# Kernel tuning notes

Measured on AMD Instinct MI355X. Metric: run time of the kernel, lower is better.

## Reference

```python
import jax, jax.numpy as jnp
import numpy as np

B, N, F, H = 4, 512, 64, 128
EPS = 0.0            # GINE eps (train_eps=False)
NEG_SLOPE = 0.01     # leaky_relu negative slope


def setup_inputs() -> dict:
    key = jax.random.key(0)
    ks = jax.random.split(key, 8)
    x = jax.random.normal(ks[0], (B, N, F), dtype=jnp.float32)
    adj = jax.random.uniform(ks[1], (B, N, N), dtype=jnp.float32)
    edge_attr = jax.random.normal(ks[2], (B, N, N, F), dtype=jnp.float32)
    mask = jax.random.randint(ks[3], (B, N), 0, 2) > 0  # bool (B,N)
    W1 = jax.random.normal(ks[4], (F, H), dtype=jnp.float32) / np.sqrt(F)
    b1 = jnp.zeros((H,), dtype=jnp.float32)
    W2 = jax.random.normal(ks[5], (H, F), dtype=jnp.float32) / np.sqrt(H)
    b2 = jnp.zeros((F,), dtype=jnp.float32)
    return {"x": x, "adj": adj, "edge_attr": edge_attr, "mask": mask,
            "W1": W1, "b1": b1, "W2": W2, "b2": b2}


def reference(x, adj, edge_attr, mask, W1, b1, W2, b2):
    # z[b,i,j,f] = x[b,i,f] + edge_attr[b,i,j,f]
    # msg = leaky_relu(adj[b,i,j] * z); aggregate over source axis i (dim 1)
    msg = jax.nn.leaky_relu(adj[..., None] * (x[:, :, None, :] + edge_attr),
                            negative_slope=NEG_SLOPE)
    agg = jnp.sum(msg, axis=1)                      # (B, N, F), indexed by j
    out = (1.0 + EPS) * x + agg                     # add_loop=True
    # nn applied on masked rows, zeros elsewhere (equivalent to out[mask]=nn(out[mask]))
    h = jax.nn.leaky_relu(out @ W1 + b1, negative_slope=NEG_SLOPE) @ W2 + b2
    return jnp.where(mask[..., None], h, jnp.zeros((), dtype=h.dtype))
```

## Files before the change

kernel.cpp:

```cpp
#include <hip/hip_runtime.h>


namespace {

constexpr int Bc = 4;
constexpr int Nc = 512;
constexpr int Fc = 64;
constexpr int Hc = 128;
constexpr int TJ = 4;
constexpr int TH = 512;
constexpr float NEG = 0.01f;

__device__ __forceinline__ float lrelu(float z) {
  return z > 0.f ? z : z * NEG;
}

__global__ __launch_bounds__(TH, 4) void gine_fused(
    const float* __restrict__ x,
    const float* __restrict__ adj,
    const float* __restrict__ ea,
    const int* __restrict__ mask,
    const float* __restrict__ W1,
    const float* __restrict__ b1,
    const float* __restrict__ W2,
    const float* __restrict__ b2,
    float* __restrict__ out)
{
  const int blk = blockIdx.x;
  const int b   = blk >> 7;
  const int j0  = (blk & 127) * TJ;
  const int tid = threadIdx.x;
  const int f4  = tid & 15;
  const int jl  = (tid >> 4) & 3;
  const int ip  = tid >> 6;

  __shared__ float4 s_adj4[Nc];
  __shared__ float4 s_part[TH];
  __shared__ float  s_out[TJ][Fc];
  __shared__ float  s_hid[TJ][Hc];

  const float* adjb = adj + (size_t)b * Nc * Nc;
  s_adj4[tid] = *reinterpret_cast<const float4*>(adjb + (size_t)tid * Nc + j0);
  __syncthreads();

  const float4* xb4 = reinterpret_cast<const float4*>(x + (size_t)b * Nc * Fc);
  const float4* eap = reinterpret_cast<const float4*>(ea)
                    + ((size_t)b * Nc * Nc + (j0 + jl)) * (Fc / 4) + f4;
  constexpr int ISTRIDE = Nc * Fc / 4;

  float4 acc = make_float4(0.f, 0.f, 0.f, 0.f);
  #pragma unroll 4
  for (int i = ip; i < Nc; i += 8) {
    const float a   = reinterpret_cast<const float*>(&s_adj4[i])[jl];
    const float4 xv = xb4[i * (Fc / 4) + f4];
    const float4 ev = eap[(size_t)i * ISTRIDE];
    acc.x += lrelu(a * (xv.x + ev.x));
    acc.y += lrelu(a * (xv.y + ev.y));
    acc.z += lrelu(a * (xv.z + ev.z));
    acc.w += lrelu(a * (xv.w + ev.w));
  }

  s_part[tid] = acc;
  __syncthreads();
  #pragma unroll
  for (int s = 256; s >= 64; s >>= 1) {
    if (tid < s) {
      float4 p = s_part[tid];
      const float4 q = s_part[tid + s];
      p.x += q.x; p.y += q.y; p.z += q.z; p.w += q.w;
      s_part[tid] = p;
    }
    __syncthreads();
  }

  if (tid < 64) {
    const int row = tid >> 4;
    const int fg  = tid & 15;
    float4 r = s_part[tid];
    const float4 xj = xb4[(j0 + row) * (Fc / 4) + fg];
    r.x += xj.x; r.y += xj.y; r.z += xj.z; r.w += xj.w;
    reinterpret_cast<float4*>(&s_out[row][0])[fg] = r;
  }
  __syncthreads();

  {
    const int row = tid >> 7;
    const int h   = tid & 127;
    float hv = b1[h];
    #pragma unroll 8
    for (int f = 0; f < Fc; ++f)
      hv = fmaf(s_out[row][f], W1[f * Hc + h], hv);
    s_hid[row][h] = lrelu(hv);
  }
  __syncthreads();

  if (tid < TJ * Fc) {
    const int row = tid >> 6;
    const int f   = tid & 63;
    float o = b2[f];
    #pragma unroll 8
    for (int h = 0; h < Hc; ++h)
      o = fmaf(s_hid[row][h], W2[h * Fc + f], o);
    const int rowg = b * Nc + j0 + row;
    out[rowg * Fc + f] = (mask[rowg] != 0) ? o : 0.f;
  }
}

}

extern "C" void kernel_launch(void* const* d_in, const int* in_sizes, int n_in,
                              void* d_out, int out_size, void* d_ws, size_t ws_size,
                              hipStream_t stream) {
  const float* x    = (const float*)d_in[0];
  const float* adj  = (const float*)d_in[1];
  const float* ea   = (const float*)d_in[2];
  const int*   mask = (const int*)d_in[3];
  const float* W1   = (const float*)d_in[4];
  const float* b1   = (const float*)d_in[5];
  const float* W2   = (const float*)d_in[6];
  const float* b2   = (const float*)d_in[7];
  float* out = (float*)d_out;

  gine_fused<<<dim3(Bc * Nc / TJ), dim3(TH), 0, stream>>>(
      x, adj, ea, mask, W1, b1, W2, b2, out);
}
```

Baseline: 378.4 us.

## Widen destination tile to eight columns with nontemporal edge loads

Doubles the number of destination columns per block (TJ 4→8). Each thread now handles 8 features as two float4 loads per source row, and the edge_attr stream uses nontemporal loads. The intent is to cut per-block overhead (adjacency staging, reduction, MLP tail), issue more memory traffic per thread, and keep the edge stream from polluting the cache. In exchange the grid halves to 256 blocks, so fewer waves are available to hide memory latency on a large GPU. Leaky-relu also becomes a branchless max.

```diff
diff --git a/kernel.cpp b/kernel.cpp
--- a/kernel.cpp
+++ b/kernel.cpp
@@ -7,15 +7,27 @@
 constexpr int Nc = 512;
 constexpr int Fc = 64;
 constexpr int Hc = 128;
-constexpr int TJ = 4;
+constexpr int TJ = 8;
 constexpr int TH = 512;
 constexpr float NEG = 0.01f;
 
+typedef float f4 __attribute__((ext_vector_type(4)));
+
 __device__ __forceinline__ float lrelu(float z) {
-  return z > 0.f ? z : z * NEG;
+  return fmaxf(z, z * NEG);
 }
 
-__global__ __launch_bounds__(TH, 4) void gine_fused(
+__device__ __forceinline__ f4 lrelu4(f4 z) {
+  f4 zn = z * NEG;
+  f4 r;
+  r.x = fmaxf(z.x, zn.x);
+  r.y = fmaxf(z.y, zn.y);
+  r.z = fmaxf(z.z, zn.z);
+  r.w = fmaxf(z.w, zn.w);
+  return r;
+}
+
+__global__ __launch_bounds__(TH, 2) void gine_fused(
     const float* __restrict__ x,
     const float* __restrict__ adj,
     const float* __restrict__ ea,
@@ -27,82 +39,100 @@
     float* __restrict__ out)
 {
   const int blk = blockIdx.x;
-  const int b   = blk >> 7;
-  const int j0  = (blk & 127) * TJ;
+  const int b   = blk >> 6;
+  const int j0  = (blk & 63) * TJ;
   const int tid = threadIdx.x;
-  const int f4  = tid & 15;
-  const int jl  = (tid >> 4) & 3;
+  const int f8  = tid & 7;
+  const int jl  = (tid >> 3) & 7;
   const int ip  = tid >> 6;
 
-  __shared__ float4 s_adj4[Nc];
-  __shared__ float4 s_part[TH];
-  __shared__ float  s_out[TJ][Fc];
-  __shared__ float  s_hid[TJ][Hc];
+  __shared__ float s_adj[Nc][TJ];
+  __shared__ f4    s_pA[TH];
+  __shared__ f4    s_pB[TH];
+  __shared__ float s_out[TJ][Fc];
+  __shared__ float s_hid[TJ][Hc];
 
   const float* adjb = adj + (size_t)b * Nc * Nc;
-  s_adj4[tid] = *reinterpret_cast<const float4*>(adjb + (size_t)tid * Nc + j0);
+  {
+    f4* s_adj4 = reinterpret_cast<f4*>(&s_adj[0][0]);
+    #pragma unroll
+    for (int k = 0; k < 2; ++k) {
+      const int fl   = tid + k * TH;
+      const int i    = fl >> 1;
+      const int half = fl & 1;
+      s_adj4[fl] = *reinterpret_cast<const f4*>(adjb + (size_t)i * Nc + j0 + half * 4);
+    }
+  }
   __syncthreads();
 
-  const float4* xb4 = reinterpret_cast<const float4*>(x + (size_t)b * Nc * Fc);
-  const float4* eap = reinterpret_cast<const float4*>(ea)
-                    + ((size_t)b * Nc * Nc + (j0 + jl)) * (Fc / 4) + f4;
-  constexpr int ISTRIDE = Nc * Fc / 4;
+  const f4* xb4 = reinterpret_cast<const f4*>(x + (size_t)b * Nc * Fc);
+  const f4* ep  = reinterpret_cast<const f4*>(ea)
+                + ((size_t)b * Nc * Nc + (size_t)(j0 + jl)) * (Fc / 4) + f8 * 2;
+  constexpr size_t ISTR = (size_t)Nc * (Fc / 4);
 
-  float4 acc = make_float4(0.f, 0.f, 0.f, 0.f);
+  f4 accA = {0.f, 0.f, 0.f, 0.f};
+  f4 accB = {0.f, 0.f, 0.f, 0.f};
   #pragma unroll 4
   for (int i = ip; i < Nc; i += 8) {
-    const float a   = reinterpret_cast<const float*>(&s_adj4[i])[jl];
-    const float4 xv = xb4[i * (Fc / 4) + f4];
-    const float4 ev = eap[(size_t)i * ISTRIDE];
-    acc.x += lrelu(a * (xv.x + ev.x));
-    acc.y += lrelu(a * (xv.y + ev.y));
-    acc.z += lrelu(a * (xv.z + ev.z));
-    acc.w += lrelu(a * (xv.w + ev.w));
+    const float a = s_adj[i][jl];
+    const f4* p  = ep + (size_t)i * ISTR;
+    const f4 e0  = __builtin_nontemporal_load(p);
+    const f4 e1  = __builtin_nontemporal_load(p + 1);
+    const f4 x0  = xb4[i * (Fc / 4) + f8 * 2];
+    const f4 x1  = xb4[i * (Fc / 4) + f8 * 2 + 1];
+    accA += lrelu4(a * (x0 + e0));
+    accB += lrelu4(a * (x1 + e1));
   }
 
-  s_part[tid] = acc;
+  s_pA[tid] = accA;
+  s_pB[tid] = accB;
   __syncthreads();
   #pragma unroll
   for (int s = 256; s >= 64; s >>= 1) {
     if (tid < s) {
-      float4 p = s_part[tid];
-      const float4 q = s_part[tid + s];
-      p.x += q.x; p.y += q.y; p.z += q.z; p.w += q.w;
-      s_part[tid] = p;
+      s_pA[tid] += s_pA[tid + s];
+      s_pB[tid] += s_pB[tid + s];
     }
     __syncthreads();
   }
 
   if (tid < 64) {
-    const int row = tid >> 4;
-    const int fg  = tid & 15;
-    float4 r = s_part[tid];
-    const float4 xj = xb4[(j0 + row) * (Fc / 4) + fg];
-    r.x += xj.x; r.y += xj.y; r.z += xj.z; r.w += xj.w;
-    reinterpret_cast<float4*>(&s_out[row][0])[fg] = r;
+    const int row = jl;
+    f4 r0 = s_pA[tid];
+    f4 r1 = s_pB[tid];
+    r0 += xb4[(j0 + row) * (Fc / 4) + f8 * 2];
+    r1 += xb4[(j0 + row) * (Fc / 4) + f8 * 2 + 1];
+    f4* so = reinterpret_cast<f4*>(&s_out[row][0]);
+    so[f8 * 2]     = r0;
+    so[f8 * 2 + 1] = r1;
   }
   __syncthreads();
 
   {
-    const int row = tid >> 7;
-    const int h   = tid & 127;
-    float hv = b1[h];
+    const int h  = tid & 127;
+    const int r0 = (tid >> 7) * 2;
+    float hv0 = b1[h];
+    float hv1 = hv0;
     #pragma unroll 8
-    for (int f = 0; f < Fc; ++f)
-      hv = fmaf(s_out[row][f], W1[f * Hc + h], hv);
-    s_hid[row][h] = lrelu(hv);
+    for (int f = 0; f < Fc; ++f) {
+      const float w = W1[f * Hc + h];
+      hv0 = fmaf(s_out[r0][f],     w, hv0);
+      hv1 = fmaf(s_out[r0 + 1][f], w, hv1);
+    }
+    s_hid[r0][h]     = lrelu(hv0);
+    s_hid[r0 + 1][h] = lrelu(hv1);
   }
   __syncthreads();
 
-  if (tid < TJ * Fc) {
+  {
+    const int f   = tid & 63;
     const int row = tid >> 6;
-    const int f   = tid & 63;
     float o = b2[f];
     #pragma unroll 8
     for (int h = 0; h < Hc; ++h)
       o = fmaf(s_hid[row][h], W2[h * Fc + f], o);
     const int rowg = b * Nc + j0 + row;
-    out[rowg * Fc + f] = (mask[rowg] != 0) ? o : 0.f;
+    out[(size_t)rowg * Fc + f] = (mask[rowg] != 0) ? o : 0.f;
   }
 }
 
```

After: 365.9 us. -3.3%, faster.
